# Performance work log

Measured on AMD Instinct MI355X. Metric: run time of the kernel, lower is better.

Reference implementation:

```python
import jax, jax.numpy as jnp
import numpy as np

IGNORE_INDEX = -100
BETA = 0.1
B, S, H, V = 8, 512, 4096, 32000


def setup_inputs() -> dict:
    key = jax.random.key(0)
    k1, k2, k3 = jax.random.split(key, 3)
    x = jax.random.normal(k1, (B, S, H), dtype=jnp.float32)
    weight = jax.random.normal(k2, (V, H), dtype=jnp.float32) * 0.02
    target = jax.random.randint(k3, (B, S), 0, V, dtype=jnp.int32)
    return {"x": x, "weight": weight, "target": target}


def reference(x, weight, target):
    len_chosen = x.shape[0] // 2
    # fused linear head: logits [B, S, V]
    logits = jnp.einsum('bsh,vh->bsv', x, weight)
    # log-softmax in fp32 as in the torch module (dtype=torch.float32)
    log_probs = jax.nn.log_softmax(logits.astype(jnp.float32), axis=-1)
    safe_tgt = jnp.clip(target, 0, V - 1)
    per_token_logps = jnp.take_along_axis(log_probs, safe_tgt[..., None].astype(jnp.int32), axis=-1)[..., 0]
    loss_mask = target != IGNORE_INDEX
    per_token_logps = jnp.where(loss_mask, per_token_logps, 0.0)
    seq_logps = per_token_logps.sum(-1)  # [B]
    # average_log_prob=True: divide by number of non-masked tokens
    seq_logps = seq_logps / loss_mask.sum(-1).astype(jnp.float32)
    policy_chosen_logps = seq_logps[:len_chosen]
    policy_rejected_logps = seq_logps[len_chosen:]
    # logits means accumulated across chunks == global means
    chosen_logits_mean = logits[:len_chosen].mean()
    rejected_logits_mean = logits[len_chosen:].mean()
    # use_ref_model=False -> reference logps are zeros
    ref_chosen = jnp.zeros_like(policy_chosen_logps)
    ref_rejected = jnp.zeros_like(policy_rejected_logps)
    # DPO preference loss
    logits_diff = BETA * ((policy_chosen_logps - ref_chosen) - (policy_rejected_logps - ref_rejected))
    preference_loss = -jax.nn.log_sigmoid(logits_diff).sum() / len_chosen
    nll_loss = jnp.zeros(())  # compute_nll_loss=False
    loss = 1.0 * nll_loss + preference_loss
    return (loss, policy_chosen_logps, policy_rejected_logps,
            chosen_logits_mean, rejected_logits_mean, nll_loss)
```

## Files before the change

### kernel.cpp

```cpp
#include <hip/hip_runtime.h>
#include <hip/hip_bf16.h>
#include <math.h>

#define IGNORE_INDEX (-100)
#define BETA 0.1f

constexpr int Mdim = 8 * 512;
constexpr int Kdim = 4096;
constexpr int Ndim = 32000;

constexpr int BM2 = 256, BN2 = 256, BK8 = 128;
constexpr int MT2 = Mdim / BM2;
constexpr int NT2 = Ndim / BN2;
constexpr int NTILES = Kdim / BK8;

constexpr int BM = 128, BN = 128;
constexpr int MT = Mdim / BM;
constexpr int NT = Ndim / BN;

typedef __bf16 bf16x8 __attribute__((ext_vector_type(8)));
typedef __bf16 bf16x4 __attribute__((ext_vector_type(4)));
typedef float  floatx4 __attribute__((ext_vector_type(4)));
typedef int    v8i __attribute__((ext_vector_type(8)));
typedef int    v4i __attribute__((ext_vector_type(4)));

#define GPTR(p) ((const __attribute__((address_space(1))) void*)(p))
#define LPTR(p) ((__attribute__((address_space(3))) void*)(p))

__global__ void cvt_f32_fp8(const float4* __restrict__ src, uint* __restrict__ dst, long n4) {
    long stride = (long)gridDim.x * blockDim.x;
    for (long i = (long)blockIdx.x * blockDim.x + threadIdx.x; i < n4; i += stride) {
        float4 a = src[i];
        int r = __builtin_amdgcn_cvt_pk_fp8_f32(a.x, a.y, 0, false);
        r     = __builtin_amdgcn_cvt_pk_fp8_f32(a.z, a.w, r, true);
        dst[i] = (uint)r;
    }
}

__global__ __launch_bounds__(512, 2)
void dpo_gemm_fp8(const unsigned char* __restrict__ x8, const unsigned char* __restrict__ w8,
                  const int* __restrict__ target,
                  float* __restrict__ sumexp, float* __restrict__ sumlog,
                  float* __restrict__ tgtlogit)
{
    __shared__ unsigned char Alds[2 * BM2 * BK8];
    __shared__ unsigned char Blds[2 * BN2 * BK8];
    __shared__ int tgt_s[BM2];

    const int tid  = threadIdx.x;
    const int lane = tid & 63;
    const int wid  = tid >> 6;
    const int wr   = wid >> 2;
    const int wc   = wid & 3;

    const int bid = blockIdx.x;
    const int swz = (bid & 7) * (MT2 * NT2 / 8) + (bid >> 3);
    const int m0  = (swz & (MT2 - 1)) * BM2;
    const int n0  = (swz / MT2) * BN2;

    if (tid < BM2) tgt_s[tid] = target[m0 + tid];

    floatx4 acc[8][4] = {};

    const int qr = lane >> 4;
    const int cr = lane & 15;

    const int srow   = lane >> 3;
    const int schunk = (lane & 7) ^ srow;
    const unsigned char* xg = x8 + (size_t)(m0 + wid * 32 + srow) * Kdim + schunk * 16;
    const unsigned char* wg = w8 + (size_t)(n0 + wid * 32 + srow) * Kdim + schunk * 16;
    const int stage_base = wid * 32 * BK8;

    #pragma unroll
    for (int i = 0; i < 4; ++i) {
        __builtin_amdgcn_global_load_lds(GPTR(xg + (size_t)i * 8 * Kdim),
                                         LPTR(Alds + stage_base + i * 1024), 16, 0, 0);
        __builtin_amdgcn_global_load_lds(GPTR(wg + (size_t)i * 8 * Kdim),
                                         LPTR(Blds + stage_base + i * 1024), 16, 0, 0);
    }
    __syncthreads();

    const int sx = cr & 7;
    const int c0 = (2 * qr) ^ sx;
    const int c1 = (2 * qr + 1) ^ sx;

    for (int t = 0; t < NTILES; ++t) {
        const int s = t & 1;
        const unsigned char* Asl = Alds + s * (BM2 * BK8);
        const unsigned char* Bsl = Blds + s * (BN2 * BK8);
        unsigned char* Asn = (unsigned char*)Alds + (s ^ 1) * (BM2 * BK8) + stage_base;
        unsigned char* Bsn = (unsigned char*)Blds + (s ^ 1) * (BN2 * BK8) + stage_base;

        v8i bfrag[4];
        #pragma unroll
        for (int ni = 0; ni < 4; ++ni) {
            const int base = (wc * 64 + ni * 16 + cr) * BK8;
            v4i lo = *(const v4i*)&Bsl[base + c0 * 16];
            v4i hi = *(const v4i*)&Bsl[base + c1 * 16];
            bfrag[ni] = __builtin_shufflevector(lo, hi, 0, 1, 2, 3, 4, 5, 6, 7);
        }

        if (t + 1 < NTILES) {
            const unsigned char* g = xg + (size_t)(t + 1) * BK8;
            #pragma unroll
            for (int i = 0; i < 4; ++i)
                __builtin_amdgcn_global_load_lds(GPTR(g + (size_t)i * 8 * Kdim),
                                                 LPTR(Asn + i * 1024), 16, 0, 0);
        }

        v8i afrag[4];
        #pragma unroll
        for (int mi = 0; mi < 4; ++mi) {
            const int base = (wr * 128 + mi * 16 + cr) * BK8;
            v4i lo = *(const v4i*)&Asl[base + c0 * 16];
            v4i hi = *(const v4i*)&Asl[base + c1 * 16];
            afrag[mi] = __builtin_shufflevector(lo, hi, 0, 1, 2, 3, 4, 5, 6, 7);
        }

        if (t + 1 < NTILES) {
            const unsigned char* g = wg + (size_t)(t + 1) * BK8;
            #pragma unroll
            for (int i = 0; i < 4; ++i)
                __builtin_amdgcn_global_load_lds(GPTR(g + (size_t)i * 8 * Kdim),
                                                 LPTR(Bsn + i * 1024), 16, 0, 0);
        }

        __builtin_amdgcn_s_setprio(1);
        #pragma unroll
        for (int mi = 0; mi < 4; ++mi)
            #pragma unroll
            for (int ni = 0; ni < 4; ++ni)
                acc[mi][ni] = __builtin_amdgcn_mfma_scale_f32_16x16x128_f8f6f4(
                    afrag[mi], bfrag[ni], acc[mi][ni],
                    0, 0, 0, 0x7F7F7F7F, 0, 0x7F7F7F7F);
        __builtin_amdgcn_s_setprio(0);

        #pragma unroll
        for (int mi = 0; mi < 4; ++mi) {
            const int base = (wr * 128 + 64 + mi * 16 + cr) * BK8;
            v4i lo = *(const v4i*)&Asl[base + c0 * 16];
            v4i hi = *(const v4i*)&Asl[base + c1 * 16];
            afrag[mi] = __builtin_shufflevector(lo, hi, 0, 1, 2, 3, 4, 5, 6, 7);
        }

        __builtin_amdgcn_s_setprio(1);
        #pragma unroll
        for (int mi = 0; mi < 4; ++mi)
            #pragma unroll
            for (int ni = 0; ni < 4; ++ni)
                acc[4 + mi][ni] = __builtin_amdgcn_mfma_scale_f32_16x16x128_f8f6f4(
                    afrag[mi], bfrag[ni], acc[4 + mi][ni],
                    0, 0, 0, 0x7F7F7F7F, 0, 0x7F7F7F7F);
        __builtin_amdgcn_s_setprio(0);

        __syncthreads();
    }

    #pragma unroll
    for (int mi8 = 0; mi8 < 8; ++mi8) {
        #pragma unroll
        for (int reg = 0; reg < 4; ++reg) {
            const int lrow = wr * 128 + mi8 * 16 + qr * 4 + reg;
            const int grow = m0 + lrow;
            const int t = tgt_s[lrow];
            float se = 0.f, sl = 0.f;
            #pragma unroll
            for (int ni = 0; ni < 4; ++ni) {
                float v = acc[mi8][ni][reg];
                int gcol = n0 + wc * 64 + ni * 16 + cr;
                if (t == gcol) tgtlogit[grow] = v;
                se += __expf(v);
                sl += v;
            }
            #pragma unroll
            for (int st = 1; st < 16; st <<= 1) {
                se += __shfl_xor(se, st, 64);
                sl += __shfl_xor(sl, st, 64);
            }
            if (cr == 0) {
                atomicAdd(&sumexp[grow], se);
                atomicAdd(&sumlog[grow], sl);
            }
        }
    }
}

__global__ __launch_bounds__(256, 2)
void dpo_gemm_f32(const float* __restrict__ x, const float* __restrict__ w,
                  const int* __restrict__ target,
                  float* __restrict__ sumexp, float* __restrict__ sumlog,
                  float* __restrict__ tgtlogit)
{
    constexpr int BK = 32;
    constexpr int LDA = 40;
    __shared__ __bf16 As[BM * LDA];
    __shared__ __bf16 Bs[BN * LDA];
    __shared__ int tgt_s[BM];

    const int tid  = threadIdx.x;
    const int lane = tid & 63;
    const int wid  = tid >> 6;
    const int wm   = wid & 1;
    const int wn   = wid >> 1;
    const int bid  = blockIdx.x;
    const int m0   = (bid & (MT - 1)) * BM;
    const int n0   = (bid / MT) * BN;

    if (tid < BM) tgt_s[tid] = target[m0 + tid];

    floatx4 acc[4][4] = {};
    const int qr = lane >> 4;
    const int cr = lane & 15;

    for (int k0 = 0; k0 < Kdim; k0 += BK) {
        __syncthreads();
        #pragma unroll
        for (int i = 0; i < 4; ++i) {
            int idx = tid + i * 256;
            int row = idx >> 3;
            int c4  = (idx & 7) * 4;
            float4 v = *(const float4*)(x + (size_t)(m0 + row) * Kdim + k0 + c4);
            bf16x4 p;
            p[0] = (__bf16)v.x; p[1] = (__bf16)v.y; p[2] = (__bf16)v.z; p[3] = (__bf16)v.w;
            *(bf16x4*)&As[row * LDA + c4] = p;
        }
        #pragma unroll
        for (int i = 0; i < 4; ++i) {
            int idx = tid + i * 256;
            int row = idx >> 3;
            int c4  = (idx & 7) * 4;
            float4 v = *(const float4*)(w + (size_t)(n0 + row) * Kdim + k0 + c4);
            bf16x4 p;
            p[0] = (__bf16)v.x; p[1] = (__bf16)v.y; p[2] = (__bf16)v.z; p[3] = (__bf16)v.w;
            *(bf16x4*)&Bs[row * LDA + c4] = p;
        }
        __syncthreads();

        bf16x8 afrag[4], bfrag[4];
        #pragma unroll
        for (int mi = 0; mi < 4; ++mi)
            afrag[mi] = *(const bf16x8*)&As[(wm * 64 + mi * 16 + cr) * LDA + qr * 8];
        #pragma unroll
        for (int ni = 0; ni < 4; ++ni)
            bfrag[ni] = *(const bf16x8*)&Bs[(wn * 64 + ni * 16 + cr) * LDA + qr * 8];

        #pragma unroll
        for (int mi = 0; mi < 4; ++mi)
            #pragma unroll
            for (int ni = 0; ni < 4; ++ni)
                acc[mi][ni] = __builtin_amdgcn_mfma_f32_16x16x32_bf16(
                    afrag[mi], bfrag[ni], acc[mi][ni], 0, 0, 0);
    }

    #pragma unroll
    for (int mi = 0; mi < 4; ++mi) {
        #pragma unroll
        for (int reg = 0; reg < 4; ++reg) {
            const int lrow = wm * 64 + mi * 16 + qr * 4 + reg;
            const int grow = m0 + lrow;
            const int t = tgt_s[lrow];
            float se = 0.f, sl = 0.f;
            #pragma unroll
            for (int ni = 0; ni < 4; ++ni) {
                float v = acc[mi][ni][reg];
                int gcol = n0 + wn * 64 + ni * 16 + cr;
                if (t == gcol) tgtlogit[grow] = v;
                se += __expf(v);
                sl += v;
            }
            #pragma unroll
            for (int st = 1; st < 16; st <<= 1) {
                se += __shfl_xor(se, st, 64);
                sl += __shfl_xor(sl, st, 64);
            }
            if (cr == 0) {
                atomicAdd(&sumexp[grow], se);
                atomicAdd(&sumlog[grow], sl);
            }
        }
    }
}

__global__ void dpo_finalize(const float* __restrict__ sumexp,
                             const float* __restrict__ sumlog,
                             const float* __restrict__ tgtlogit,
                             const int* __restrict__ target,
                             float* __restrict__ out)
{
    __shared__ float s_logp[8], s_sl[8];
    const int lane = threadIdx.x & 63;
    const int w    = threadIdx.x >> 6;

    float lp = 0.f, cnt = 0.f, sl = 0.f;
    #pragma unroll
    for (int i = 0; i < 8; ++i) {
        int t  = w * 512 + i * 64 + lane;
        int tg = target[t];
        if (tg != IGNORE_INDEX) {
            lp  += tgtlogit[t] - logf(sumexp[t]);
            cnt += 1.f;
        }
        sl += sumlog[t];
    }
    #pragma unroll
    for (int s = 1; s < 64; s <<= 1) {
        lp  += __shfl_xor(lp, s, 64);
        cnt += __shfl_xor(cnt, s, 64);
        sl  += __shfl_xor(sl, s, 64);
    }
    if (lane == 0) { s_logp[w] = lp / cnt; s_sl[w] = sl; }
    __syncthreads();

    if (threadIdx.x == 0) {
        float cm = 0.f, rm = 0.f, loss = 0.f;
        for (int i = 0; i < 4; ++i) { cm += s_sl[i]; rm += s_sl[4 + i]; }
        const float denom = 4.f * 512.f * 32000.f;
        cm /= denom; rm /= denom;
        for (int i = 0; i < 4; ++i) {
            float d = BETA * (s_logp[i] - s_logp[4 + i]);
            float l = (d > 0.f) ? log1pf(expf(-d)) : (-d + log1pf(expf(d)));
            loss += l;
        }
        loss *= 0.25f;
        out[0] = loss;
        for (int i = 0; i < 4; ++i) out[1 + i] = s_logp[i];
        for (int i = 0; i < 4; ++i) out[5 + i] = s_logp[4 + i];
        out[9]  = cm;
        out[10] = rm;
        out[11] = 0.f;
    }
}

extern "C" void kernel_launch(void* const* d_in, const int* in_sizes, int n_in,
                              void* d_out, int out_size, void* d_ws, size_t ws_size,
                              hipStream_t stream) {
    const float* x      = (const float*)d_in[0];
    const float* wgt    = (const float*)d_in[1];
    const int*   target = (const int*)d_in[2];
    float* out = (float*)d_out;

    float* sumexp   = (float*)d_ws;
    float* sumlog   = sumexp + Mdim;
    float* tgtlogit = sumlog + Mdim;
    char*  base     = (char*)d_ws + 3 * Mdim * sizeof(float);
    unsigned char* x8 = (unsigned char*)base;
    unsigned char* w8 = x8 + (size_t)Mdim * Kdim;

    const size_t ws_needed = 3 * Mdim * sizeof(float)
                           + (size_t)Mdim * Kdim
                           + (size_t)Ndim * Kdim;

    hipMemsetAsync(d_ws, 0, 2 * Mdim * sizeof(float), stream);

    if (ws_size >= ws_needed) {
        const long nx4 = (long)Mdim * Kdim / 4;
        const long nw4 = (long)Ndim * Kdim / 4;
        int bx = (int)(((nx4 + 255) / 256) < 2048 ? ((nx4 + 255) / 256) : 2048);
        int bw = (int)(((nw4 + 255) / 256) < 2048 ? ((nw4 + 255) / 256) : 2048);
        cvt_f32_fp8<<<bx, 256, 0, stream>>>((const float4*)x,   (uint*)x8, nx4);
        cvt_f32_fp8<<<bw, 256, 0, stream>>>((const float4*)wgt, (uint*)w8, nw4);
        dpo_gemm_fp8<<<MT2 * NT2, 512, 0, stream>>>(x8, w8, target, sumexp, sumlog, tgtlogit);
    } else {
        dpo_gemm_f32<<<MT * NT, 256, 0, stream>>>(x, wgt, target, sumexp, sumlog, tgtlogit);
    }
    dpo_finalize<<<1, 512, 0, stream>>>(sumexp, sumlog, tgtlogit, target, out);
}
```

Baseline: 1.309 ms.

## Split FP8 GEMM k-loop into barrier-synced MFMA phases and merge conversion kernels

Restructures the FP8 GEMM main loop into four phases that each load two A fragments and then issue eight MFMAs. The phases are separated by raw s_barrier, explicit waitcnt and sched_barrier, in place of one large fragment load per half and a trailing __syncthreads. The intent is to interleave LDS reads, global prefetch and MFMA issue more finely across waves, with vmcnt waits placed only at tile end. It also merges the two fp32-to-fp8 conversion launches into one grid-stride kernel to save a launch. The extra barriers add synchronisation cost, and the hand-placed waitcnts carry a correctness risk.

```diff
diff --git a/kernel.cpp b/kernel.cpp
--- a/kernel.cpp
+++ b/kernel.cpp
@@ -27,13 +27,17 @@
 #define GPTR(p) ((const __attribute__((address_space(1))) void*)(p))
 #define LPTR(p) ((__attribute__((address_space(3))) void*)(p))
 
-__global__ void cvt_f32_fp8(const float4* __restrict__ src, uint* __restrict__ dst, long n4) {
+__global__ void cvt_f32_fp8(const float4* __restrict__ xs, uint* __restrict__ xd, long nx4,
+                            const float4* __restrict__ ws, uint* __restrict__ wd, long nw4) {
     long stride = (long)gridDim.x * blockDim.x;
-    for (long i = (long)blockIdx.x * blockDim.x + threadIdx.x; i < n4; i += stride) {
-        float4 a = src[i];
+    long ntot = nx4 + nw4;
+    for (long i = (long)blockIdx.x * blockDim.x + threadIdx.x; i < ntot; i += stride) {
+        const float4* s; uint* d; long j;
+        if (i < nx4) { s = xs; d = xd; j = i; } else { s = ws; d = wd; j = i - nx4; }
+        float4 a = s[j];
         int r = __builtin_amdgcn_cvt_pk_fp8_f32(a.x, a.y, 0, false);
         r     = __builtin_amdgcn_cvt_pk_fp8_f32(a.z, a.w, r, true);
-        dst[i] = (uint)r;
+        d[j] = (uint)r;
     }
 }
 
@@ -78,20 +82,23 @@
         __builtin_amdgcn_global_load_lds(GPTR(wg + (size_t)i * 8 * Kdim),
                                          LPTR(Blds + stage_base + i * 1024), 16, 0, 0);
     }
-    __syncthreads();
+    asm volatile("s_waitcnt vmcnt(0)" ::: "memory");
+    __builtin_amdgcn_s_barrier();
+    asm volatile("" ::: "memory");
 
     const int sx = cr & 7;
     const int c0 = (2 * qr) ^ sx;
     const int c1 = (2 * qr + 1) ^ sx;
 
     for (int t = 0; t < NTILES; ++t) {
-        const int s = t & 1;
-        const unsigned char* Asl = Alds + s * (BM2 * BK8);
-        const unsigned char* Bsl = Blds + s * (BN2 * BK8);
-        unsigned char* Asn = (unsigned char*)Alds + (s ^ 1) * (BM2 * BK8) + stage_base;
-        unsigned char* Bsn = (unsigned char*)Blds + (s ^ 1) * (BN2 * BK8) + stage_base;
-
-        v8i bfrag[4];
+        const unsigned char* Asl = Alds + (t & 1) * (BM2 * BK8);
+        const unsigned char* Bsl = Blds + (t & 1) * (BN2 * BK8);
+        unsigned char* Asn = (unsigned char*)Alds + ((t + 1) & 1) * (BM2 * BK8) + stage_base;
+        unsigned char* Bsn = (unsigned char*)Blds + ((t + 1) & 1) * (BN2 * BK8) + stage_base;
+        const bool pf = (t + 1 < NTILES);
+
+        v8i bfrag[4], af0, af1;
+
         #pragma unroll
         for (int ni = 0; ni < 4; ++ni) {
             const int base = (wc * 64 + ni * 16 + cr) * BK8;
@@ -99,61 +106,124 @@
             v4i hi = *(const v4i*)&Bsl[base + c1 * 16];
             bfrag[ni] = __builtin_shufflevector(lo, hi, 0, 1, 2, 3, 4, 5, 6, 7);
         }
-
-        if (t + 1 < NTILES) {
+        {
+            const int ba = (wr * 128 + 0 * 16 + cr) * BK8;
+            v4i lo = *(const v4i*)&Asl[ba + c0 * 16];
+            v4i hi = *(const v4i*)&Asl[ba + c1 * 16];
+            af0 = __builtin_shufflevector(lo, hi, 0, 1, 2, 3, 4, 5, 6, 7);
+            const int bb = (wr * 128 + 1 * 16 + cr) * BK8;
+            v4i lo2 = *(const v4i*)&Asl[bb + c0 * 16];
+            v4i hi2 = *(const v4i*)&Asl[bb + c1 * 16];
+            af1 = __builtin_shufflevector(lo2, hi2, 0, 1, 2, 3, 4, 5, 6, 7);
+        }
+        if (pf) {
             const unsigned char* g = xg + (size_t)(t + 1) * BK8;
             #pragma unroll
             for (int i = 0; i < 4; ++i)
                 __builtin_amdgcn_global_load_lds(GPTR(g + (size_t)i * 8 * Kdim),
                                                  LPTR(Asn + i * 1024), 16, 0, 0);
         }
-
-        v8i afrag[4];
-        #pragma unroll
-        for (int mi = 0; mi < 4; ++mi) {
-            const int base = (wr * 128 + mi * 16 + cr) * BK8;
-            v4i lo = *(const v4i*)&Asl[base + c0 * 16];
-            v4i hi = *(const v4i*)&Asl[base + c1 * 16];
-            afrag[mi] = __builtin_shufflevector(lo, hi, 0, 1, 2, 3, 4, 5, 6, 7);
-        }
-
-        if (t + 1 < NTILES) {
+        __builtin_amdgcn_s_barrier();
+        asm volatile("s_waitcnt lgkmcnt(0)" ::: "memory");
+        __builtin_amdgcn_sched_barrier(0);
+        __builtin_amdgcn_s_setprio(1);
+        #pragma unroll
+        for (int ni = 0; ni < 4; ++ni) {
+            acc[0][ni] = __builtin_amdgcn_mfma_scale_f32_16x16x128_f8f6f4(
+                af0, bfrag[ni], acc[0][ni], 0, 0, 0, 0x7F7F7F7F, 0, 0x7F7F7F7F);
+            acc[1][ni] = __builtin_amdgcn_mfma_scale_f32_16x16x128_f8f6f4(
+                af1, bfrag[ni], acc[1][ni], 0, 0, 0, 0x7F7F7F7F, 0, 0x7F7F7F7F);
+        }
+        __builtin_amdgcn_s_setprio(0);
+        __builtin_amdgcn_sched_barrier(0);
+        __builtin_amdgcn_s_barrier();
+        asm volatile("" ::: "memory");
+
+        {
+            const int ba = (wr * 128 + 2 * 16 + cr) * BK8;
+            v4i lo = *(const v4i*)&Asl[ba + c0 * 16];
+            v4i hi = *(const v4i*)&Asl[ba + c1 * 16];
+            af0 = __builtin_shufflevector(lo, hi, 0, 1, 2, 3, 4, 5, 6, 7);
+            const int bb = (wr * 128 + 3 * 16 + cr) * BK8;
+            v4i lo2 = *(const v4i*)&Asl[bb + c0 * 16];
+            v4i hi2 = *(const v4i*)&Asl[bb + c1 * 16];
+            af1 = __builtin_shufflevector(lo2, hi2, 0, 1, 2, 3, 4, 5, 6, 7);
+        }
+        if (pf) {
             const unsigned char* g = wg + (size_t)(t + 1) * BK8;
             #pragma unroll
             for (int i = 0; i < 4; ++i)
                 __builtin_amdgcn_global_load_lds(GPTR(g + (size_t)i * 8 * Kdim),
                                                  LPTR(Bsn + i * 1024), 16, 0, 0);
         }
-
+        __builtin_amdgcn_s_barrier();
+        asm volatile("s_waitcnt lgkmcnt(0)" ::: "memory");
+        __builtin_amdgcn_sched_barrier(0);
         __builtin_amdgcn_s_setprio(1);
         #pragma unroll
-        for (int mi = 0; mi < 4; ++mi)
-            #pragma unroll
-            for (int ni = 0; ni < 4; ++ni)
-                acc[mi][ni] = __builtin_amdgcn_mfma_scale_f32_16x16x128_f8f6f4(
-                    afrag[mi], bfrag[ni], acc[mi][ni],
-                    0, 0, 0, 0x7F7F7F7F, 0, 0x7F7F7F7F);
+        for (int ni = 0; ni < 4; ++ni) {
+            acc[2][ni] = __builtin_amdgcn_mfma_scale_f32_16x16x128_f8f6f4(
+                af0, bfrag[ni], acc[2][ni], 0, 0, 0, 0x7F7F7F7F, 0, 0x7F7F7F7F);
+            acc[3][ni] = __builtin_amdgcn_mfma_scale_f32_16x16x128_f8f6f4(
+                af1, bfrag[ni], acc[3][ni], 0, 0, 0, 0x7F7F7F7F, 0, 0x7F7F7F7F);
+        }
         __builtin_amdgcn_s_setprio(0);
-
-        #pragma unroll
-        for (int mi = 0; mi < 4; ++mi) {
-            const int base = (wr * 128 + 64 + mi * 16 + cr) * BK8;
-            v4i lo = *(const v4i*)&Asl[base + c0 * 16];
-            v4i hi = *(const v4i*)&Asl[base + c1 * 16];
-            afrag[mi] = __builtin_shufflevector(lo, hi, 0, 1, 2, 3, 4, 5, 6, 7);
-        }
-
+        __builtin_amdgcn_sched_barrier(0);
+        __builtin_amdgcn_s_barrier();
+        asm volatile("" ::: "memory");
+
+        {
+            const int ba = (wr * 128 + 4 * 16 + cr) * BK8;
+            v4i lo = *(const v4i*)&Asl[ba + c0 * 16];
+            v4i hi = *(const v4i*)&Asl[ba + c1 * 16];
+            af0 = __builtin_shufflevector(lo, hi, 0, 1, 2, 3, 4, 5, 6, 7);
+            const int bb = (wr * 128 + 5 * 16 + cr) * BK8;
+            v4i lo2 = *(const v4i*)&Asl[bb + c0 * 16];
+            v4i hi2 = *(const v4i*)&Asl[bb + c1 * 16];
+            af1 = __builtin_shufflevector(lo2, hi2, 0, 1, 2, 3, 4, 5, 6, 7);
+        }
+        __builtin_amdgcn_s_barrier();
+        asm volatile("s_waitcnt lgkmcnt(0)" ::: "memory");
+        __builtin_amdgcn_sched_barrier(0);
         __builtin_amdgcn_s_setprio(1);
         #pragma unroll
-        for (int mi = 0; mi < 4; ++mi)
-            #pragma unroll
-            for (int ni = 0; ni < 4; ++ni)
-                acc[4 + mi][ni] = __builtin_amdgcn_mfma_scale_f32_16x16x128_f8f6f4(
-                    afrag[mi], bfrag[ni], acc[4 + mi][ni],
-                    0, 0, 0, 0x7F7F7F7F, 0, 0x7F7F7F7F);
+        for (int ni = 0; ni < 4; ++ni) {
+            acc[4][ni] = __builtin_amdgcn_mfma_scale_f32_16x16x128_f8f6f4(
+                af0, bfrag[ni], acc[4][ni], 0, 0, 0, 0x7F7F7F7F, 0, 0x7F7F7F7F);
+            acc[5][ni] = __builtin_amdgcn_mfma_scale_f32_16x16x128_f8f6f4(
+                af1, bfrag[ni], acc[5][ni], 0, 0, 0, 0x7F7F7F7F, 0, 0x7F7F7F7F);
+        }
         __builtin_amdgcn_s_setprio(0);
-
-        __syncthreads();
+        __builtin_amdgcn_sched_barrier(0);
+        __builtin_amdgcn_s_barrier();
+        asm volatile("" ::: "memory");
+
+        {
+            const int ba = (wr * 128 + 6 * 16 + cr) * BK8;
+            v4i lo = *(const v4i*)&Asl[ba + c0 * 16];
+            v4i hi = *(const v4i*)&Asl[ba + c1 * 16];
+            af0 = __builtin_shufflevector(lo, hi, 0, 1, 2, 3, 4, 5, 6, 7);
+            const int bb = (wr * 128 + 7 * 16 + cr) * BK8;
+            v4i lo2 = *(const v4i*)&Asl[bb + c0 * 16];
+            v4i hi2 = *(const v4i*)&Asl[bb + c1 * 16];
+            af1 = __builtin_shufflevector(lo2, hi2, 0, 1, 2, 3, 4, 5, 6, 7);
+        }
+        __builtin_amdgcn_s_barrier();
+        asm volatile("s_waitcnt lgkmcnt(0)" ::: "memory");
+        __builtin_amdgcn_sched_barrier(0);
+        __builtin_amdgcn_s_setprio(1);
+        #pragma unroll
+        for (int ni = 0; ni < 4; ++ni) {
+            acc[6][ni] = __builtin_amdgcn_mfma_scale_f32_16x16x128_f8f6f4(
+                af0, bfrag[ni], acc[6][ni], 0, 0, 0, 0x7F7F7F7F, 0, 0x7F7F7F7F);
+            acc[7][ni] = __builtin_amdgcn_mfma_scale_f32_16x16x128_f8f6f4(
+                af1, bfrag[ni], acc[7][ni], 0, 0, 0, 0x7F7F7F7F, 0, 0x7F7F7F7F);
+        }
+        __builtin_amdgcn_s_setprio(0);
+        __builtin_amdgcn_sched_barrier(0);
+        asm volatile("s_waitcnt vmcnt(0)" ::: "memory");
+        __builtin_amdgcn_s_barrier();
+        asm volatile("" ::: "memory");
     }
 
     #pragma unroll
@@ -355,10 +425,8 @@
     if (ws_size >= ws_needed) {
         const long nx4 = (long)Mdim * Kdim / 4;
         const long nw4 = (long)Ndim * Kdim / 4;
-        int bx = (int)(((nx4 + 255) / 256) < 2048 ? ((nx4 + 255) / 256) : 2048);
-        int bw = (int)(((nw4 + 255) / 256) < 2048 ? ((nw4 + 255) / 256) : 2048);
-        cvt_f32_fp8<<<bx, 256, 0, stream>>>((const float4*)x,   (uint*)x8, nx4);
-        cvt_f32_fp8<<<bw, 256, 0, stream>>>((const float4*)wgt, (uint*)w8, nw4);
+        cvt_f32_fp8<<<2048, 256, 0, stream>>>((const float4*)x, (uint*)x8, nx4,
+                                              (const float4*)wgt, (uint*)w8, nw4);
         dpo_gemm_fp8<<<MT2 * NT2, 512, 0, stream>>>(x8, w8, target, sumexp, sumlog, tgtlogit);
     } else {
         dpo_gemm_f32<<<MT * NT, 256, 0, stream>>>(x, wgt, target, sumexp, sumlog, tgtlogit);
```

Result: slower. 1.387 ms (+6.0%).
